# Performance work log

Measured on AMD Instinct MI355X. Metric: run time of the kernel, lower is better.

The kernel has to match this reference:

```python
import jax, jax.numpy as jnp
import numpy as np

# config
H = 1536; NH = 12; NKV = 4; D = H // NH
E = 8; TOPK = 2; I_EXP = 512; I_SH = 1024
B = 2; S = 2048; MAXPOS = 4096
SCALE = 0.0078125; RESM = 0.22; EPS = 1e-6
NEG = -1e30


def setup_inputs() -> dict:
    key = jax.random.key(0)
    ks = jax.random.split(key, 16)
    w = lambda k, shape: jax.random.normal(k, shape, dtype=jnp.float32) * 0.02
    # real RoPE tables: cos/sin over [MAXPOS, D]
    inv_freq = 1.0 / (10000.0 ** (jnp.arange(0, D, 2, dtype=jnp.float32) / D))
    freqs = jnp.outer(jnp.arange(MAXPOS, dtype=jnp.float32), inv_freq)
    emb = jnp.concatenate([freqs, freqs], axis=-1)  # [MAXPOS, D]
    return {
        'hidden_states': jax.random.normal(ks[0], (B, S, H), dtype=jnp.float32),
        'position_ids': jnp.broadcast_to(jnp.arange(S, dtype=jnp.int32)[None, :], (B, S)),
        'cos': jnp.cos(emb), 'sin': jnp.sin(emb),
        'ln1_w': jnp.ones((H,), jnp.float32), 'ln2_w': jnp.ones((H,), jnp.float32),
        'wq': w(ks[1], (NH * D, H)), 'wk': w(ks[2], (NKV * D, H)),
        'wv': w(ks[3], (NKV * D, H)), 'wo': w(ks[4], (H, NH * D)),
        'router_w': w(ks[5], (E, H)),
        'w_gate': w(ks[6], (E, I_EXP, H)), 'w_up': w(ks[7], (E, I_EXP, H)),
        'w_down': w(ks[8], (E, H, I_EXP)),
        'shared_in': w(ks[9], (2 * I_SH, H)), 'shared_out': w(ks[10], (H, I_SH)),
    }


def _rmsnorm(x, w):
    xf = x.astype(jnp.float32)
    v = jnp.mean(xf * xf, axis=-1, keepdims=True)
    return (w * (xf * jax.lax.rsqrt(v + EPS))).astype(x.dtype)


def _rotate_half(x):
    x1, x2 = jnp.split(x, 2, axis=-1)
    return jnp.concatenate([-x2, x1], axis=-1)


def reference(hidden_states, position_ids, cos, sin, ln1_w, ln2_w, wq, wk, wv, wo,
              router_w, w_gate, w_up, w_down, shared_in, shared_out):
    b, s, h = hidden_states.shape
    # --- attention block with pre-RMSNorm ---
    residual = hidden_states
    x = _rmsnorm(hidden_states, ln1_w)
    q = (x @ wq.T).reshape(b, s, NH, D)
    k = (x @ wk.T).reshape(b, s, NKV, D)
    v = (x @ wv.T).reshape(b, s, NKV, D)
    c = cos[position_ids][:, :, None, :]  # [B,S,1,D] (unsqueeze_dim=2, bsnd)
    sn = sin[position_ids][:, :, None, :]
    q = q * c + _rotate_half(q) * sn
    k = k * c + _rotate_half(k) * sn
    rep = NH // NKV  # GQA: repeat kv heads
    k = jnp.repeat(k, rep, axis=2)
    v = jnp.repeat(v, rep, axis=2)
    scores = jnp.einsum('bqhd,bkhd->bhqk', q, k) * SCALE
    causal = jnp.tril(jnp.ones((s, s), dtype=bool))
    probs = jax.nn.softmax(jnp.where(causal, scores, NEG), axis=-1)
    attn = jnp.einsum('bhqk,bkhd->bqhd', probs, v).reshape(b, s, h)
    hidden = residual + (attn @ wo.T) * RESM
    # --- MoE + shared MLP with pre-RMSNorm ---
    residual = hidden
    x2 = _rmsnorm(hidden, ln2_w)
    tok = x2.reshape(-1, h)  # [T,H]
    T = tok.shape[0]
    logits = (tok @ router_w.T).astype(jnp.float32)  # [T,E]
    top_logits, top_idx = jax.lax.top_k(logits, TOPK)
    rw = jax.nn.softmax(top_logits, axis=-1).astype(tok.dtype)  # [T,K]
    # dense-expert evaluation combined with sparse routing weights (same math as torch_moe)
    g = jnp.einsum('th,eih->tei', tok, w_gate)
    u = jnp.einsum('th,eih->tei', tok, w_up)
    ye = jnp.einsum('tei,ehi->teh', jax.nn.silu(g) * u, w_down)  # [T,E,H]
    combine = jnp.zeros((T, E), dtype=tok.dtype).at[jnp.arange(T)[:, None], top_idx].add(rw)
    moe_out = jnp.einsum('te,teh->th', combine, ye)
    a, bgate = jnp.split(tok @ shared_in.T, 2, axis=-1)
    shared = (jax.nn.silu(a) * bgate) @ shared_out.T
    ffn = (moe_out + shared).reshape(b, s, h)
    return residual + ffn * RESM
```

## Files before the change

kernel.cpp:

```cpp
#include <hip/hip_runtime.h>
#include <cstdint>
#include <cstddef>

using u16 = unsigned short;
using u32 = unsigned int;

typedef __bf16 bf16x8 __attribute__((ext_vector_type(8)));
typedef float  f32x4  __attribute__((ext_vector_type(4)));

#define DI __device__ __forceinline__

constexpr int Hdim = 1536;
constexpr int NHq = 12, NKVh = 4, Dh = 128;
constexpr int NE = 8, IEXP = 512, ISH = 1024;
constexpr int Bn = 2, Sn = 2048, Tn = Bn * Sn;
constexpr float RESM = 0.22f;

DI float bf2f(u16 u) { union { u32 i; float f; } c; c.i = (u32)u << 16; return c.f; }
DI u16 f2bf(float f) {
  union { float f; u32 i; } c; c.f = f;
  u32 r = c.i + 0x7fffu + ((c.i >> 16) & 1u);
  return (u16)(r >> 16);
}

DI void gl2lds16(const u16* g, u16* l) {
  __builtin_amdgcn_global_load_lds((__attribute__((address_space(1))) void*)g,
                                   (__attribute__((address_space(3))) void*)l, 16, 0, 0);
}

__constant__ signed char c_qt2[24] = {7,8,9,10,11,12,13,14,15,15,6,14,5,13,4,12,3,11,2,10,1,9,0,8};
__constant__ signed char c_ch[24]  = {0,0,0,0,0,0,0,0,0,1, 0,1, 0,1, 0,1, 0,1, 0,1, 0,1, 0,1};

constexpr long B0 = 589824;
constexpr long B1 = B0 + 196608;
constexpr long B2 = B1 + 196608;
constexpr long B3 = B2 + 589824;
constexpr long B4 = B3 + 3145728;
constexpr long B5 = B4 + 1572864;
constexpr long B6 = B5 + 786432;
constexpr long B7 = B6 + 393216;

__global__ void cvt_all_k(const float4* __restrict__ wq, const float4* __restrict__ wk,
                          const float4* __restrict__ wv, const float4* __restrict__ wo,
                          const float4* __restrict__ wg, const float4* __restrict__ wu,
                          const float4* __restrict__ wd, const float4* __restrict__ wsi,
                          const float4* __restrict__ wso,
                          ushort4* __restrict__ qkvb, ushort4* __restrict__ wob,
                          ushort4* __restrict__ wgub, ushort4* __restrict__ wdnb,
                          ushort4* __restrict__ wsib, ushort4* __restrict__ wsob) {
  long i = (long)blockIdx.x * 256 + threadIdx.x;
  float4 v; ushort4* dst;
  if (i < B0) { v = wq[i]; dst = qkvb + i; }
  else if (i < B1) { v = wk[i - B0]; dst = qkvb + i; }
  else if (i < B2) { v = wv[i - B1]; dst = qkvb + i; }
  else if (i < B3) { v = wo[i - B2]; dst = wob + (i - B2); }
  else if (i < B4) {
    long k = i - B3;
    long e = k / 393216, rem = k % 393216;
    long r = rem / 384, h4 = rem % 384;
    v = (r < 512) ? wg[(e * 512 + r) * 384 + h4] : wu[(e * 512 + (r - 512)) * 384 + h4];
    dst = wgub + k;
  }
  else if (i < B5) { v = wd[i - B4]; dst = wdnb + (i - B4); }
  else if (i < B6) { v = wsi[i - B5]; dst = wsib + (i - B5); }
  else { v = wso[i - B6]; dst = wsob + (i - B6); }
  *dst = ushort4{f2bf(v.x), f2bf(v.y), f2bf(v.z), f2bf(v.w)};
}


__global__ void rmsnorm_k(const float* __restrict__ x, const float* __restrict__ w, u16* __restrict__ o) {
  __shared__ float red[4];
  long t = blockIdx.x;
  const float* row = x + t * Hdim;
  float ss = 0.f;
  for (int i = threadIdx.x; i < Hdim; i += 256) { float v = row[i]; ss += v * v; }
#pragma unroll
  for (int m = 32; m >= 1; m >>= 1) ss += __shfl_xor(ss, m);
  if ((threadIdx.x & 63) == 0) red[threadIdx.x >> 6] = ss;
  __syncthreads();
  float tot = red[0] + red[1] + red[2] + red[3];
  float sc = rsqrtf(tot * (1.f / Hdim) + 1e-6f);
  for (int i = threadIdx.x; i < Hdim; i += 256) o[t * Hdim + i] = f2bf(row[i] * sc * w[i]);
}

__global__ void rope_k(const u16* __restrict__ qkv, const int* __restrict__ pos,
                       const float* __restrict__ cosT, const float* __restrict__ sinT,
                       u16* __restrict__ qb, u16* __restrict__ kb) {
  int t = blockIdx.x;
  int b = t >> 11, s = t & 2047;
  int p = pos[t];
  const u16* row = qkv + (long)t * 2560;
  const float* cp = cosT + (long)p * Dh;
  const float* sp = sinT + (long)p * Dh;
  for (int idx = threadIdx.x; idx < NHq * Dh; idx += 256) {
    int hh = idx >> 7, d = idx & 127;
    float x = bf2f(row[idx]);
    float xr = (d < 64) ? -bf2f(row[hh * 128 + d + 64]) : bf2f(row[hh * 128 + d - 64]);
    float v = x * cp[d] + xr * sp[d];
    qb[((long)(b * NHq + hh) * Sn + s) * Dh + d] = f2bf(v * 0.0078125f);
  }
  for (int idx = threadIdx.x; idx < NKVh * Dh; idx += 256) {
    int hh = idx >> 7, d = idx & 127;
    float x = bf2f(row[1536 + idx]);
    float xr = (d < 64) ? -bf2f(row[1536 + hh * 128 + d + 64]) : bf2f(row[1536 + hh * 128 + d - 64]);
    float v = x * cp[d] + xr * sp[d];
    kb[((long)(b * NKVh + hh) * Sn + s) * Dh + d] = f2bf(v);
  }
}

__global__ void vt_k(const u16* __restrict__ qkv, u16* __restrict__ vt) {
  __shared__ __align__(16) u16 tile[64][72];
  const int s0 = blockIdx.x * 64, d0 = blockIdx.y * 64, bh = blockIdx.z;
  const int b = bh >> 2, hk = bh & 3;
  const int tid = threadIdx.x;
#pragma unroll
  for (int ph = 0; ph < 2; ph++) {
    int e = ph * 256 + tid;
    int r = e >> 3, c = e & 7;
    uint4 v = *(const uint4*)(qkv + (long)(b * Sn + s0 + r) * 2560 + 2048 + hk * 128 + d0 + c * 8);
    *(uint4*)&tile[r][c * 8] = v;
  }
  __syncthreads();
#pragma unroll
  for (int ph = 0; ph < 2; ph++) {
    int e = ph * 256 + tid;
    int rr = e >> 3, cc = e & 7;
    union { uint4 v; u16 s[8]; } tmp;
#pragma unroll
    for (int i = 0; i < 8; i++) tmp.s[i] = tile[cc * 8 + i][rr];
    *(uint4*)(vt + ((long)(bh * Dh) + d0 + rr) * Sn + s0 + cc * 8) = tmp.v;
  }
}

__global__ void router_k(const float* __restrict__ hid2, const float* __restrict__ ln2,
                         const float* __restrict__ rw,
                         int* __restrict__ tidx, float* __restrict__ tw) {
  int wid = threadIdx.x >> 6, lane = threadIdx.x & 63;
  long t = (long)blockIdx.x * 4 + wid;
  const float* x = hid2 + t * Hdim;
  float xv[24];
  float ss = 0.f;
#pragma unroll
  for (int i = 0; i < 24; i++) { float v = x[lane + i * 64]; xv[i] = v; ss += v * v; }
#pragma unroll
  for (int m = 32; m >= 1; m >>= 1) ss += __shfl_xor(ss, m);
  float sc = rsqrtf(ss * (1.f / Hdim) + 1e-6f);
#pragma unroll
  for (int i = 0; i < 24; i++) xv[i] = xv[i] * sc * ln2[lane + i * 64];
  float lg[8];
  for (int e = 0; e < 8; e++) {
    const float* wrow = rw + e * Hdim;
    float s = 0.f;
#pragma unroll
    for (int i = 0; i < 24; i++) s += xv[i] * wrow[lane + i * 64];
#pragma unroll
    for (int m = 32; m >= 1; m >>= 1) s += __shfl_xor(s, m);
    lg[e] = s;
  }
  if (lane == 0) {
    int i0 = 0; float b0 = lg[0];
    for (int e = 1; e < 8; e++) if (lg[e] > b0) { b0 = lg[e]; i0 = e; }
    int i1 = -1; float b1 = -3e38f;
    for (int e = 0; e < 8; e++) if (e != i0 && lg[e] > b1) { b1 = lg[e]; i1 = e; }
    float w1 = 1.f / (1.f + __expf(b0 - b1));
    float w0 = 1.f - w1;
    tidx[2 * t] = i0; tidx[2 * t + 1] = i1;
    tw[2 * t] = w0; tw[2 * t + 1] = w1;
  }
}

__global__ void route_scan_k(const int* __restrict__ tidx, const float* __restrict__ tw,
                             int* __restrict__ perm, float* __restrict__ slotw,
                             int* __restrict__ tokslot, int* __restrict__ counts,
                             int* __restrict__ seg) {
  __shared__ int pref[8][257];
  __shared__ int segs[8];
  const int tid = threadIdx.x;
  const int base = tid * 32;
  int le[32];
#pragma unroll
  for (int j = 0; j < 32; j++) le[j] = tidx[base + j];
#pragma unroll
  for (int e = 0; e < 8; e++) {
    int c = 0;
#pragma unroll
    for (int j = 0; j < 32; j++) c += (le[j] == e) ? 1 : 0;
    pref[e][tid + 1] = c;
  }
  if (tid < 8) pref[tid][0] = 0;
  __syncthreads();
  if (tid < 8) {
    int acc = 0;
    for (int t2 = 0; t2 < 256; t2++) { acc += pref[tid][t2 + 1]; pref[tid][t2 + 1] = acc; }
    counts[tid] = acc;
  }
  __syncthreads();
  if (tid == 0) {
    int acc = 0;
    for (int e = 0; e < 8; e++) { segs[e] = acc; seg[e] = acc; acc += pref[e][256]; }
  }
  __syncthreads();
#pragma unroll
  for (int j = 0; j < 32; j++) {
    int e = le[j];
    int rank = 0;
#pragma unroll
    for (int j2 = 0; j2 < 32; j2++)
      if (j2 < j) rank += (le[j2] == e) ? 1 : 0;
    int p = segs[e] + pref[e][tid] + rank;
    perm[p] = (base + j) >> 1;
    slotw[p] = tw[base + j];
    tokslot[base + j] = p;
  }
}

__global__ void act_moe_k(const u16* __restrict__ gu, const float* __restrict__ slotw,
                          u16* __restrict__ act) {
  long i8 = (long)blockIdx.x * 256 + threadIdx.x;
  if (i8 >= (long)2 * Tn * IEXP / 8) return;
  long slot = i8 / 64; int c8 = (int)(i8 % 64);
  union { uint4 v; u16 s[8]; } gv, uv, ov;
  gv.v = *(const uint4*)(gu + slot * 1024 + c8 * 8);
  uv.v = *(const uint4*)(gu + slot * 1024 + 512 + c8 * 8);
  float sw = slotw[slot];
#pragma unroll
  for (int k = 0; k < 8; k++) {
    float g = bf2f(gv.s[k]), u = bf2f(uv.s[k]);
    ov.s[k] = f2bf((g / (1.f + __expf(-g))) * u * sw);
  }
  *(uint4*)(act + i8 * 8) = ov.v;
}

__global__ void act_sh_k(const u16* __restrict__ shr, u16* __restrict__ act) {
  long i8 = (long)blockIdx.x * 256 + threadIdx.x;
  if (i8 >= (long)Tn * ISH / 8) return;
  long t = i8 / 128; int c8 = (int)(i8 % 128);
  union { uint4 v; u16 s[8]; } av, bv, ov;
  av.v = *(const uint4*)(shr + t * 2048 + c8 * 8);
  bv.v = *(const uint4*)(shr + t * 2048 + 1024 + c8 * 8);
#pragma unroll
  for (int k = 0; k < 8; k++) {
    float a = bf2f(av.s[k]), b = bf2f(bv.s[k]);
    ov.s[k] = f2bf((a / (1.f + __expf(-a))) * b);
  }
  *(uint4*)(act + i8 * 8) = ov.v;
}

__global__ void final_k(const float* __restrict__ hidden2, const u16* __restrict__ shy,
                        const u16* __restrict__ Y, const int* __restrict__ tokslot,
                        float* __restrict__ out) {
  long i4 = (long)blockIdx.x * 256 + threadIdx.x;
  if (i4 >= (long)Tn * Hdim / 4) return;
  long t = i4 / 384; int h4 = (int)(i4 % 384);
  long s0 = tokslot[2 * t], s1 = tokslot[2 * t + 1];
  float4 hv = *(const float4*)(hidden2 + i4 * 4);
  ushort4 sv = *(const ushort4*)(shy + i4 * 4);
  ushort4 y0 = *(const ushort4*)(Y + s0 * Hdim + h4 * 4);
  ushort4 y1 = *(const ushort4*)(Y + s1 * Hdim + h4 * 4);
  float4 r;
  r.x = hv.x + (bf2f(sv.x) + bf2f(y0.x) + bf2f(y1.x)) * RESM;
  r.y = hv.y + (bf2f(sv.y) + bf2f(y0.y) + bf2f(y1.y)) * RESM;
  r.z = hv.z + (bf2f(sv.z) + bf2f(y0.z) + bf2f(y1.z)) * RESM;
  r.w = hv.w + (bf2f(sv.w) + bf2f(y0.w) + bf2f(y1.w)) * RESM;
  *(float4*)(out + i4 * 4) = r;
}

template <int EPI>
__global__ __launch_bounds__(256) void gemm_bt(
    const u16* __restrict__ A, const u16* __restrict__ Bb,
    float* __restrict__ Cf, u16* __restrict__ Cb, const float* __restrict__ res,
    const int* __restrict__ perm, const int* __restrict__ counts, const int* __restrict__ segoff,
    int M, int N, int K, long bstride) {
  __shared__ __align__(16) u16 smem[8448];
  u16* As = smem;
  u16* Bs = smem + 4096;
  const int e = blockIdx.z;
  const u16* Bp = Bb + (long)e * bstride;
  const int meff = counts ? counts[e] : M;
  const int base = segoff ? segoff[e] : 0;
  const int m0 = blockIdx.y * 128;
  if (m0 >= meff) return;
  const int n0 = blockIdx.x * 128;
  const int tid = threadIdx.x;
  const int lane = tid & 63, wid = tid >> 6;
  const int l15 = lane & 15, quad = lane >> 4;
  const int wm = wid & 1, wn = wid >> 1;

  const int r0 = tid >> 2, c0 = (tid & 3) * 8;
  int g0 = m0 + r0; if (g0 >= meff) g0 = meff - 1;
  int g1 = m0 + r0 + 64; if (g1 >= meff) g1 = meff - 1;
  const long arow0 = perm ? (long)perm[base + g0] : (long)(base + g0);
  const long arow1 = perm ? (long)perm[base + g1] : (long)(base + g1);
  const long brow0 = n0 + r0, brow1 = n0 + r0 + 64;

  f32x4 acc[4][4];
#pragma unroll
  for (int i = 0; i < 4; i++)
#pragma unroll
    for (int j = 0; j < 4; j++) acc[i][j] = f32x4{0.f, 0.f, 0.f, 0.f};

  for (int k0 = 0; k0 < K; k0 += 32) {
    __syncthreads();
    gl2lds16(A + arow0 * K + k0 + c0, &As[tid * 8]);
    gl2lds16(A + arow1 * K + k0 + c0, &As[(tid + 256) * 8]);
    gl2lds16(Bp + brow0 * K + k0 + c0, &Bs[tid * 8]);
    gl2lds16(Bp + brow1 * K + k0 + c0, &Bs[(tid + 256) * 8]);
    __syncthreads();
    bf16x8 af[4], bfr[4];
#pragma unroll
    for (int i = 0; i < 4; i++) af[i] = *(const bf16x8*)&As[(wm * 64 + i * 16 + l15) * 32 + quad * 8];
#pragma unroll
    for (int j = 0; j < 4; j++) bfr[j] = *(const bf16x8*)&Bs[(wn * 64 + j * 16 + l15) * 32 + quad * 8];
#pragma unroll
    for (int i = 0; i < 4; i++)
#pragma unroll
      for (int j = 0; j < 4; j++)
        acc[i][j] = __builtin_amdgcn_mfma_f32_16x16x32_bf16(af[i], bfr[j], acc[i][j], 0, 0, 0);
  }

  __syncthreads();
  if (EPI == 0) {
    u16* sT = smem;
#pragma unroll
    for (int half = 0; half < 2; half++) {
      if (wm == half) {
#pragma unroll
        for (int i = 0; i < 4; i++)
#pragma unroll
          for (int j = 0; j < 4; j++)
#pragma unroll
            for (int r = 0; r < 4; r++)
              sT[(i * 16 + quad * 4 + r) * 132 + wn * 64 + j * 16 + l15] = f2bf(acc[i][j][r]);
      }
      __syncthreads();
#pragma unroll
      for (int rep = 0; rep < 4; rep++) {
        int lr = rep * 16 + (tid >> 4);
        int gm = m0 + half * 64 + lr;
        if (gm < meff) {
          int ch = (tid & 15) * 8;
          uint4 v = *(const uint4*)&sT[lr * 132 + ch];
          *(uint4*)(Cb + (long)(base + gm) * N + n0 + ch) = v;
        }
      }
      __syncthreads();
    }
  } else {
    float* sF = (float*)smem;
#pragma unroll
    for (int ph = 0; ph < 4; ph++) {
      if (wm == (ph >> 1)) {
#pragma unroll
        for (int ii = 0; ii < 2; ii++) {
          int i = (ph & 1) * 2 + ii;
#pragma unroll
          for (int j = 0; j < 4; j++)
#pragma unroll
            for (int r = 0; r < 4; r++)
              sF[(ii * 16 + quad * 4 + r) * 132 + wn * 64 + j * 16 + l15] = acc[i][j][r];
        }
      }
      __syncthreads();
#pragma unroll
      for (int rep = 0; rep < 2; rep++) {
        int lr = rep * 16 + (tid >> 4);
        int gm = m0 + ph * 32 + lr;
        if (gm < meff) {
          int ch = (tid & 15) * 8;
          long idx = (long)(base + gm) * N + n0 + ch;
          float4 a0 = *(const float4*)&sF[lr * 132 + ch];
          float4 a1 = *(const float4*)&sF[lr * 132 + ch + 4];
          float4 r0v = *(const float4*)&res[idx];
          float4 r1v = *(const float4*)&res[idx + 4];
          float4 o0v{r0v.x + a0.x * RESM, r0v.y + a0.y * RESM, r0v.z + a0.z * RESM, r0v.w + a0.w * RESM};
          float4 o1v{r1v.x + a1.x * RESM, r1v.y + a1.y * RESM, r1v.z + a1.z * RESM, r1v.w + a1.w * RESM};
          *(float4*)&Cf[idx] = o0v;
          *(float4*)&Cf[idx + 4] = o1v;
        }
      }
      __syncthreads();
    }
  }
}

__global__ __launch_bounds__(256, 2) void flash7_k(
    const u16* __restrict__ qb, const u16* __restrict__ kb, const u16* __restrict__ vt,
    u16* __restrict__ o0, u16* __restrict__ o1,
    float* __restrict__ ls0, float* __restrict__ ls1,
    u16* __restrict__ attn) {
  __shared__ __align__(16) u16 smem[37376];
  const int rnk = blockIdx.x / 24, bh = blockIdx.x % 24;
  const int qt2 = c_qt2[rnk], ch = c_ch[rnk];
  const int jmaxall = 2 * qt2 + 1;
  const int kt0 = ch ? 16 : 0;
  const int ktend = ch ? jmaxall : (jmaxall < 15 ? jmaxall : 15);
  const int tc = ktend - kt0 + 1;
  const bool split = (qt2 >= 8);
  const int b = bh / 12, h = bh % 12, hk = h / 3;
  const int q0 = qt2 * 128;
  const u16* Q = qb + (long)(b * NHq + h) * Sn * Dh;
  const u16* Kp = kb + (long)(b * NKVh + hk) * Sn * Dh;
  const u16* Vp = vt + (long)(b * NKVh + hk) * Dh * Sn;
  const int tid = threadIdx.x, lane = tid & 63, wid = tid >> 6;
  const int l15 = lane & 15, quad = lane >> 4;

  bf16x8 qf[2][4];
#pragma unroll
  for (int s = 0; s < 2; s++) {
    const u16* qr = Q + (long)(q0 + s * 64 + wid * 16 + l15) * Dh + quad * 8;
#pragma unroll
    for (int ks = 0; ks < 4; ks++) qf[s][ks] = *(const bf16x8*)(qr + ks * 32);
  }

  int koff[4], voff[4];
#pragma unroll
  for (int i = 0; i < 4; i++) {
    int krow = wid * 16 + i * 4 + (lane >> 4);
    int kch = (lane & 15) ^ ((i * 4 + (lane >> 4)) & 15);
    koff[i] = krow * 128 + kch * 8;
    int vrow = wid * 32 + i * 8 + (lane >> 3);
    int vch = (lane & 7) ^ (lane >> 3);
    voff[i] = vch * 8;
    voff[i] |= vrow << 16;
  }

  auto stage = [&](int kt, int buf) {
    u16* kd = smem + buf * 8192;
    u16* vd = smem + 16384 + buf * 8192;
    const u16* ksrc = Kp + (long)kt * 64 * 128;
#pragma unroll
    for (int i = 0; i < 4; i++) {
      gl2lds16(ksrc + koff[i], kd + (wid * 16 + i * 4) * 128);
      int vrow = voff[i] >> 16, vcol = voff[i] & 0xffff;
      gl2lds16(Vp + (long)vrow * Sn + kt * 64 + vcol, vd + (wid * 32 + i * 8) * 64);
    }
  };

  f32x4 o[2][8];
#pragma unroll
  for (int s = 0; s < 2; s++)
#pragma unroll
    for (int i = 0; i < 8; i++) o[s][i] = f32x4{0.f, 0.f, 0.f, 0.f};
  float lsum[2][4] = {{0.f, 0.f, 0.f, 0.f}, {0.f, 0.f, 0.f, 0.f}};

  stage(kt0, 0);
  __syncthreads();

  for (int j = 0; j < tc; j++) {
    const int kt = kt0 + j;
    const int A = j & 1;
    if (j + 1 < tc) stage(kt + 1, A ^ 1);
    const u16* sKc = smem + A * 8192;
    const u16* sVc = smem + 16384 + A * 8192;
    u16* sP = smem + 32768;
    const bool do0 = (kt <= 2 * qt2);

    f32x4 sv0[4], sv1[4];
#pragma unroll
    for (int nt = 0; nt < 4; nt++) { sv0[nt] = f32x4{0.f, 0.f, 0.f, 0.f}; sv1[nt] = f32x4{0.f, 0.f, 0.f, 0.f}; }
#pragma unroll
    for (int ks = 0; ks < 4; ks++)
#pragma unroll
      for (int nt = 0; nt < 4; nt++) {
        bf16x8 bk = *(const bf16x8*)&sKc[(nt * 16 + l15) * 128 + (((ks * 4 + quad) ^ l15) & 15) * 8];
        if (do0) sv0[nt] = __builtin_amdgcn_mfma_f32_16x16x32_bf16(qf[0][ks], bk, sv0[nt], 0, 0, 0);
        sv1[nt] = __builtin_amdgcn_mfma_f32_16x16x32_bf16(qf[1][ks], bk, sv1[nt], 0, 0, 0);
      }
    if (kt == 2 * qt2) {
#pragma unroll
      for (int nt = 0; nt < 4; nt++)
#pragma unroll
        for (int r = 0; r < 4; r++) {
          int rr = q0 + wid * 16 + quad * 4 + r, cc = kt * 64 + nt * 16 + l15;
          if (cc > rr) sv0[nt][r] = -1e30f;
        }
    }
    if (kt == jmaxall) {
#pragma unroll
      for (int nt = 0; nt < 4; nt++)
#pragma unroll
        for (int r = 0; r < 4; r++) {
          int rr = q0 + 64 + wid * 16 + quad * 4 + r, cc = kt * 64 + nt * 16 + l15;
          if (cc > rr) sv1[nt][r] = -1e30f;
        }
    }
#pragma unroll
    for (int s = 0; s < 2; s++) {
      if (s == 0 && !do0) continue;
      const f32x4* sv = (s == 0) ? sv0 : sv1;
#pragma unroll
      for (int nt = 0; nt < 4; nt++)
#pragma unroll
        for (int r = 0; r < 4; r++) {
          float pe = __expf(sv[nt][r]);
          lsum[s][r] += pe;
          sP[(wid * 16 + quad * 4 + r) * 72 + nt * 16 + l15] = f2bf(pe);
        }
#pragma unroll
      for (int ks = 0; ks < 2; ks++) {
        bf16x8 pa = *(const bf16x8*)&sP[(wid * 16 + l15) * 72 + ks * 32 + quad * 8];
#pragma unroll
        for (int dt = 0; dt < 8; dt++) {
          bf16x8 vv = *(const bf16x8*)&sVc[(dt * 16 + l15) * 64 + (((ks * 4 + quad) ^ (l15 & 7)) & 7) * 8];
          o[s][dt] = __builtin_amdgcn_mfma_f32_16x16x32_bf16(pa, vv, o[s][dt], 0, 0, 0);
        }
      }
    }
    __syncthreads();
  }

  float rs[2][4];
#pragma unroll
  for (int s = 0; s < 2; s++)
#pragma unroll
    for (int r = 0; r < 4; r++) {
      float t = lsum[s][r];
      t += __shfl_xor(t, 1); t += __shfl_xor(t, 2); t += __shfl_xor(t, 4); t += __shfl_xor(t, 8);
      rs[s][r] = t;
    }
  u16* sT = smem;
#pragma unroll
  for (int s = 0; s < 2; s++) {
    float iv[4];
#pragma unroll
    for (int r = 0; r < 4; r++) iv[r] = split ? 1.f : 1.f / rs[s][r];
#pragma unroll
    for (int dt = 0; dt < 8; dt++)
#pragma unroll
      for (int r = 0; r < 4; r++)
        sT[(wid * 16 + quad * 4 + r) * 132 + dt * 16 + l15] = f2bf(o[s][dt][r] * iv[r]);
    __syncthreads();
    if (!split) {
#pragma unroll
      for (int rep = 0; rep < 4; rep++) {
        int row = rep * 16 + (tid >> 4);
        int c8 = (tid & 15) * 8;
        uint4 v = *(const uint4*)&sT[row * 132 + c8];
        *(uint4*)(attn + ((long)(b * Sn + q0 + s * 64 + row)) * (long)Hdim + h * Dh + c8) = v;
      }
    } else {
      u16* op = (ch == 0 ? o0 : o1) + ((long)bh * Sn + q0 + s * 64) * Dh;
#pragma unroll
      for (int rep = 0; rep < 4; rep++) {
        int row = rep * 16 + (tid >> 4);
        int c8 = (tid & 15) * 8;
        uint4 v = *(const uint4*)&sT[row * 132 + c8];
        *(uint4*)(op + (long)row * Dh + c8) = v;
      }
    }
    __syncthreads();
  }
  if (split && l15 == 0) {
    float* lp = (ch == 0 ? ls0 : ls1) + (long)bh * Sn + q0;
#pragma unroll
    for (int s = 0; s < 2; s++)
#pragma unroll
      for (int r = 0; r < 4; r++) lp[s * 64 + wid * 16 + quad * 4 + r] = rs[s][r];
  }
}

__global__ void attn_norm6_k(const u16* __restrict__ o0, const u16* __restrict__ o1,
                             const float* __restrict__ l0, const float* __restrict__ l1,
                             u16* __restrict__ attn) {
  const int gid = blockIdx.x;
  const int bh = gid >> 6, rb = gid & 63;
  const int row = 1024 + rb * 16 + (threadIdx.x >> 4);
  const int ch = (threadIdx.x & 15) * 8;
  const long idx = ((long)bh * Sn + row) * Dh + ch;
  union { uint4 v; u16 s[8]; } a, b2, ov;
  a.v = *(const uint4*)(o0 + idx);
  b2.v = *(const uint4*)(o1 + idx);
  const float inv = 1.f / (l0[(long)bh * Sn + row] + l1[(long)bh * Sn + row]);
#pragma unroll
  for (int k = 0; k < 8; k++) ov.s[k] = f2bf((bf2f(a.s[k]) + bf2f(b2.s[k])) * inv);
  const int b = bh / 12, h = bh % 12;
  *(uint4*)(attn + ((long)(b * Sn + row)) * (long)Hdim + h * Dh + ch) = ov.v;
}


extern "C" void kernel_launch(void* const* d_in, const int* in_sizes, int n_in,
                              void* d_out, int out_size, void* d_ws, size_t ws_size,
                              hipStream_t stream) {
  const float* hidden = (const float*)d_in[0];
  const int* pos = (const int*)d_in[1];
  const float* cosT = (const float*)d_in[2];
  const float* sinT = (const float*)d_in[3];
  const float* ln1 = (const float*)d_in[4];
  const float* ln2 = (const float*)d_in[5];
  const float* wq = (const float*)d_in[6];
  const float* wk = (const float*)d_in[7];
  const float* wv = (const float*)d_in[8];
  const float* wo = (const float*)d_in[9];
  const float* router_w = (const float*)d_in[10];
  const float* w_gate = (const float*)d_in[11];
  const float* w_up = (const float*)d_in[12];
  const float* w_down = (const float*)d_in[13];
  const float* shared_in = (const float*)d_in[14];
  const float* shared_out = (const float*)d_in[15];
  float* out = (float*)d_out;

  char* p = (char*)d_ws;
  auto alloc = [&](size_t bytes) -> char* {
    char* r = p; p += (bytes + 255) & ~(size_t)255; return r;
  };
  u16* wqkv_b = (u16*)alloc((size_t)2560 * Hdim * 2);
  u16* wo_b = (u16*)alloc((size_t)Hdim * Hdim * 2);
  u16* wgu_b = (u16*)alloc((size_t)NE * 1024 * Hdim * 2);
  u16* wdown_b = (u16*)alloc((size_t)NE * Hdim * IEXP * 2);
  u16* wshin_b = (u16*)alloc((size_t)2048 * Hdim * 2);
  u16* wshout_b = (u16*)alloc((size_t)Hdim * ISH * 2);
  char* regH = alloc((size_t)Tn * Hdim * 4);
  char* reg1 = alloc((size_t)Tn * 2560 * 2);
  char* reg2 = alloc((size_t)Bn * NHq * Sn * Dh * 2);
  char* reg3 = alloc((size_t)2 * Bn * NKVh * Sn * Dh * 2);
  u16* Y_b = (u16*)alloc((size_t)2 * Tn * Hdim * 2);
  int* tidx = (int*)alloc(Tn * 2 * 4);
  float* tw = (float*)alloc(Tn * 2 * 4);
  int* tokslot = (int*)alloc(Tn * 2 * 4);
  int* perm = (int*)alloc(Tn * 2 * 4);
  float* slotw = (float*)alloc(Tn * 2 * 4);
  int* counts = (int*)alloc(64);
  int* seg = (int*)alloc(64);
  float* lsum0 = (float*)alloc((size_t)24 * Sn * 4);
  float* lsum1 = (float*)alloc((size_t)24 * Sn * 4);

  u16* x1n = (u16*)regH;
  float* hidden2 = (float*)regH;
  u16* opart0 = (u16*)regH;
  u16* opart1 = (u16*)Y_b;
  u16* qkvraw = (u16*)reg1;
  u16* attn = (u16*)reg1;
  u16* gu_b = (u16*)reg1;
  u16* shraw_b = (u16*)reg1;
  u16* qbuf = (u16*)reg2;
  u16* x2n = (u16*)reg2;
  u16* shy_b = (u16*)reg2;
  u16* kbuf = (u16*)reg3;
  u16* vtbuf = kbuf + (size_t)Bn * NKVh * Sn * Dh;
  u16* act_b = (u16*)reg3;
  u16* shact_b = (u16*)reg3;

  auto cdiv = [](long a, long b) { return (int)((a + b - 1) / b); };

  cvt_all_k<<<(int)(B7 / 256), 256, 0, stream>>>(
      (const float4*)wq, (const float4*)wk, (const float4*)wv, (const float4*)wo,
      (const float4*)w_gate, (const float4*)w_up, (const float4*)w_down,
      (const float4*)shared_in, (const float4*)shared_out,
      (ushort4*)wqkv_b, (ushort4*)wo_b, (ushort4*)wgu_b, (ushort4*)wdown_b,
      (ushort4*)wshin_b, (ushort4*)wshout_b);

  rmsnorm_k<<<Tn, 256, 0, stream>>>(hidden, ln1, x1n);
  gemm_bt<0><<<dim3(2560 / 128, Tn / 128, 1), 256, 0, stream>>>(
      x1n, wqkv_b, nullptr, qkvraw, nullptr, nullptr, nullptr, nullptr, Tn, 2560, Hdim, 0);
  rope_k<<<Tn, 256, 0, stream>>>(qkvraw, pos, cosT, sinT, qbuf, kbuf);
  vt_k<<<dim3(Sn / 64, Dh / 64, Bn * NKVh), 256, 0, stream>>>(qkvraw, vtbuf);
  flash7_k<<<dim3(576, 1, 1), 256, 0, stream>>>(qbuf, kbuf, vtbuf, opart0, opart1, lsum0, lsum1, attn);
  attn_norm6_k<<<dim3(24 * 64, 1, 1), 256, 0, stream>>>(opart0, opart1, lsum0, lsum1, attn);
  gemm_bt<2><<<dim3(Hdim / 128, Tn / 128, 1), 256, 0, stream>>>(
      attn, wo_b, hidden2, nullptr, hidden, nullptr, nullptr, nullptr, Tn, Hdim, Hdim, 0);

  rmsnorm_k<<<Tn, 256, 0, stream>>>(hidden2, ln2, x2n);
  router_k<<<Tn / 4, 256, 0, stream>>>(hidden2, ln2, router_w, tidx, tw);
  route_scan_k<<<1, 256, 0, stream>>>(tidx, tw, perm, slotw, tokslot, counts, seg);
  gemm_bt<0><<<dim3(1024 / 128, Tn / 128, NE), 256, 0, stream>>>(
      x2n, wgu_b, nullptr, gu_b, nullptr, perm, counts, seg, 0, 1024, Hdim, (long)1024 * Hdim);
  act_moe_k<<<cdiv((long)2 * Tn * IEXP / 8, 256), 256, 0, stream>>>(gu_b, slotw, act_b);
  gemm_bt<0><<<dim3(Hdim / 128, Tn / 128, NE), 256, 0, stream>>>(
      act_b, wdown_b, nullptr, Y_b, nullptr, nullptr, counts, seg, 0, Hdim, IEXP, (long)Hdim * IEXP);

  gemm_bt<0><<<dim3(2048 / 128, Tn / 128, 1), 256, 0, stream>>>(
      x2n, wshin_b, nullptr, shraw_b, nullptr, nullptr, nullptr, nullptr, Tn, 2048, Hdim, 0);
  act_sh_k<<<cdiv((long)Tn * ISH / 8, 256), 256, 0, stream>>>(shraw_b, shact_b);
  gemm_bt<0><<<dim3(Hdim / 128, Tn / 128, 1), 256, 0, stream>>>(
      shact_b, wshout_b, nullptr, shy_b, nullptr, nullptr, nullptr, nullptr, Tn, Hdim, ISH, 0);

  final_k<<<cdiv((long)Tn * Hdim / 4, 256), 256, 0, stream>>>(hidden2, shy_b, Y_b, tokslot, out);
}
```

Measured before the change: 590.3 us.

## Double-buffer GEMM LDS tiles and swizzle workgroups across XCDs

The GEMM main loop now uses two LDS buffers: it issues the global-to-LDS loads for the next K-slice before computing on the current one and needs only one barrier per iteration, so load latency can overlap MFMA work. Workgroup IDs are also remapped so consecutive tiles land on the same XCD, which is meant to improve L2 reuse of A/B rows. Shared memory doubles to 32KB per block, which may reduce occupancy. The one-barrier scheme relies on the async LDS writes being complete by the next barrier.

```diff
diff --git a/kernel.cpp b/kernel.cpp
--- a/kernel.cpp
+++ b/kernel.cpp
@@ -271,16 +271,21 @@
     float* __restrict__ Cf, u16* __restrict__ Cb, const float* __restrict__ res,
     const int* __restrict__ perm, const int* __restrict__ counts, const int* __restrict__ segoff,
     int M, int N, int K, long bstride) {
-  __shared__ __align__(16) u16 smem[8448];
-  u16* As = smem;
-  u16* Bs = smem + 4096;
+  __shared__ __align__(16) u16 smem[16384];
   const int e = blockIdx.z;
   const u16* Bp = Bb + (long)e * bstride;
   const int meff = counts ? counts[e] : M;
   const int base = segoff ? segoff[e] : 0;
-  const int m0 = blockIdx.y * 128;
+
+  const int nwg = gridDim.x * gridDim.y;
+  const int orig = blockIdx.y * gridDim.x + blockIdx.x;
+  const int qq = nwg >> 3, rr8 = nwg & 7;
+  const int xcd = orig & 7, lin = orig >> 3;
+  const int swz = (xcd < rr8 ? xcd * (qq + 1) : rr8 * (qq + 1) + (xcd - rr8) * qq) + lin;
+  const int m0 = (swz / gridDim.x) * 128;
   if (m0 >= meff) return;
-  const int n0 = blockIdx.x * 128;
+  const int n0 = (swz % gridDim.x) * 128;
+
   const int tid = threadIdx.x;
   const int lane = tid & 63, wid = tid >> 6;
   const int l15 = lane & 15, quad = lane >> 4;
@@ -299,26 +304,37 @@
 #pragma unroll
     for (int j = 0; j < 4; j++) acc[i][j] = f32x4{0.f, 0.f, 0.f, 0.f};
 
-  for (int k0 = 0; k0 < K; k0 += 32) {
-    __syncthreads();
-    gl2lds16(A + arow0 * K + k0 + c0, &As[tid * 8]);
-    gl2lds16(A + arow1 * K + k0 + c0, &As[(tid + 256) * 8]);
-    gl2lds16(Bp + brow0 * K + k0 + c0, &Bs[tid * 8]);
-    gl2lds16(Bp + brow1 * K + k0 + c0, &Bs[(tid + 256) * 8]);
-    __syncthreads();
+  const int nst = K >> 5;
+  auto stageAB = [&](int t, int buf) {
+    const int k0 = t << 5;
+    u16* Ad = smem + buf * 8192;
+    u16* Bd = Ad + 4096;
+    gl2lds16(A + arow0 * K + k0 + c0, &Ad[tid * 8]);
+    gl2lds16(A + arow1 * K + k0 + c0, &Ad[(tid + 256) * 8]);
+    gl2lds16(Bp + brow0 * K + k0 + c0, &Bd[tid * 8]);
+    gl2lds16(Bp + brow1 * K + k0 + c0, &Bd[(tid + 256) * 8]);
+  };
+
+  stageAB(0, 0);
+  __syncthreads();
+  for (int t = 0; t < nst; t++) {
+    const int cur = t & 1;
+    if (t + 1 < nst) stageAB(t + 1, cur ^ 1);
+    const u16* Asc = smem + cur * 8192;
+    const u16* Bsc = Asc + 4096;
     bf16x8 af[4], bfr[4];
 #pragma unroll
-    for (int i = 0; i < 4; i++) af[i] = *(const bf16x8*)&As[(wm * 64 + i * 16 + l15) * 32 + quad * 8];
-#pragma unroll
-    for (int j = 0; j < 4; j++) bfr[j] = *(const bf16x8*)&Bs[(wn * 64 + j * 16 + l15) * 32 + quad * 8];
+    for (int i = 0; i < 4; i++) af[i] = *(const bf16x8*)&Asc[(wm * 64 + i * 16 + l15) * 32 + quad * 8];
+#pragma unroll
+    for (int j = 0; j < 4; j++) bfr[j] = *(const bf16x8*)&Bsc[(wn * 64 + j * 16 + l15) * 32 + quad * 8];
 #pragma unroll
     for (int i = 0; i < 4; i++)
 #pragma unroll
       for (int j = 0; j < 4; j++)
         acc[i][j] = __builtin_amdgcn_mfma_f32_16x16x32_bf16(af[i], bfr[j], acc[i][j], 0, 0, 0);
-  }
-
-  __syncthreads();
+    __syncthreads();
+  }
+
   if (EPI == 0) {
     u16* sT = smem;
 #pragma unroll
```

Measured after the change: 666.4 us. 1.13x slower.
